# Performance work log

Hardware: AMD Instinct MI355X
Metric: run time of the kernel (lower is better)

Reference implementation:

```python
import jax, jax.numpy as jnp
import numpy as np

B, L, D, H = 4, 2048, 1024, 64  # batch, seq, d_model, head_size

def setup_inputs() -> dict:
    key = jax.random.key(0)
    k1, k2 = jax.random.split(key)
    x = jax.random.normal(k1, (B, L, D), dtype=jnp.float32)
    # nn.Linear(d_model, head_size, bias=False) weight: [head_size, d_model]
    Wq = jax.random.normal(k2, (H, D), dtype=jnp.float32) * (1.0 / np.sqrt(D))
    return {"x": x, "Wq": Wq}

def reference(x, Wq):
    # Faithful to source bug: q, k, v ALL use the query projection.
    q = jnp.einsum('bld,hd->blh', x, Wq)
    k = q
    v = q
    d_k = x.shape[-1]  # source uses d_model, not head_size
    scores = jnp.einsum('blh,bmh->blm', q, k) / jnp.sqrt(jnp.float32(d_k))
    Lq = x.shape[1]
    causal = jnp.tril(jnp.ones((Lq, Lq), dtype=bool))
    scores = jnp.where(causal, scores, -jnp.inf)
    attn = jax.nn.softmax(scores, axis=-1)
    # dropout in eval mode -> identity
    return jnp.einsum('blm,bmh->blh', attn, v)
```

## Files before the change

### kernel.cpp

```cpp
#include <hip/hip_runtime.h>
#include <cmath>

#define Bb 4
#define Ll 2048
#define Dd 1024
#define Hh 64

typedef float f32x4 __attribute__((ext_vector_type(4)));
typedef short s16x8 __attribute__((ext_vector_type(8)));

#if __has_builtin(__builtin_amdgcn_exp2f)
#define EXP2(x) __builtin_amdgcn_exp2f(x)
#else
#define EXP2(x) exp2f(x)
#endif
#define SCL 0.0450842200278f

__device__ __forceinline__ unsigned short f2bf(float f) {
    union { float f; unsigned int u; } v; v.f = f;
    unsigned int u = v.u;
    return (unsigned short)((u + 0x7FFFu + ((u >> 16) & 1u)) >> 16);
}
__device__ __forceinline__ unsigned int pack2(float a, float b) {
    return (unsigned int)f2bf(a) | ((unsigned int)f2bf(b) << 16);
}

__global__ __launch_bounds__(256) void wq_cvt(const float* __restrict__ Wq,
                                              unsigned short* __restrict__ wqb) {
    const int i = (blockIdx.x * 256 + threadIdx.x) * 8;
    float4 a = *(const float4*)(Wq + i);
    float4 b = *(const float4*)(Wq + i + 4);
    uint4 p; p.x = pack2(a.x, a.y); p.y = pack2(a.z, a.w);
    p.z = pack2(b.x, b.y); p.w = pack2(b.z, b.w);
    *(uint4*)(wqb + i) = p;
}

__global__ __launch_bounds__(128) void proj_mfma(const float* __restrict__ x,
                                                 const unsigned short* __restrict__ wqb,
                                                 unsigned short* __restrict__ q,
                                                 unsigned short* __restrict__ qT) {
    const int t = threadIdx.x;
    const int lane = t & 63;
    const int wv = t >> 6;
    const int m15 = lane & 15, q_ = lane >> 4;
    const int row0 = blockIdx.x * 32 + wv * 16;
    const float* xr = x + (size_t)(row0 + m15) * Dd + q_ * 8;

    f32x4 acc[4];
#pragma unroll
    for (int i = 0; i < 4; ++i) acc[i] = (f32x4){0.f, 0.f, 0.f, 0.f};

#pragma unroll 4
    for (int ks = 0; ks < 32; ++ks) {
        float4 a = *(const float4*)(xr + ks * 32);
        float4 b = *(const float4*)(xr + ks * 32 + 4);
        union { s16x8 v; uint4 u; } A;
        A.u.x = pack2(a.x, a.y); A.u.y = pack2(a.z, a.w);
        A.u.z = pack2(b.x, b.y); A.u.w = pack2(b.z, b.w);
#pragma unroll
        for (int ct = 0; ct < 4; ++ct) {
            s16x8 B = *(const s16x8*)(wqb + (size_t)(ct * 16 + m15) * Dd + ks * 32 + q_ * 8);
            acc[ct] = __builtin_amdgcn_mfma_f32_16x16x32_bf16(A.v, B, acc[ct], 0, 0, 0);
        }
    }
    const int b = row0 >> 11;
    const int mloc = (row0 & 2047) + q_ * 4;
#pragma unroll
    for (int ct = 0; ct < 4; ++ct) {
        const int h = ct * 16 + m15;
        unsigned short u0 = f2bf(acc[ct][0]), u1 = f2bf(acc[ct][1]);
        unsigned short u2 = f2bf(acc[ct][2]), u3 = f2bf(acc[ct][3]);
        q[(size_t)(row0 + q_ * 4 + 0) * Hh + h] = u0;
        q[(size_t)(row0 + q_ * 4 + 1) * Hh + h] = u1;
        q[(size_t)(row0 + q_ * 4 + 2) * Hh + h] = u2;
        q[(size_t)(row0 + q_ * 4 + 3) * Hh + h] = u3;
        ushort4 pk; pk.x = u0; pk.y = u1; pk.z = u2; pk.w = u3;
        *(ushort4*)&qT[((size_t)(b * Hh + h)) * Ll + mloc] = pk;
    }
}

__global__ __launch_bounds__(256, 3) void flash_mfma(const unsigned short* __restrict__ qg,
                                                     const unsigned short* __restrict__ qTg,
                                                     float* __restrict__ PO,
                                                     float* __restrict__ ML) {
    const int i = blockIdx.x;
    const int b = blockIdx.y;
    int g = (int)((sqrtf(1.0f + 2.0f * (float)i) - 1.0f) * 0.5f);
    while (2 * g * (g + 1) > i) --g;
    while (2 * (g + 1) * (g + 2) <= i) ++g;
    const int r_ = i - 2 * g * (g + 1);
    const int qt = 4 * g + r_ / (g + 1);
    const int s  = r_ % (g + 1);

    __shared__ uint4 Qs4[512], Ks4[512], Vt4[512];
    __shared__ __align__(16) unsigned short Pb[4 * 16 * 72];
    const int t = threadIdx.x, lane = t & 63, w = t >> 6;
    const int m15 = lane & 15, q_ = lane >> 4;
    const unsigned short* qb  = qg  + (size_t)b * Ll * Hh;
    const unsigned short* qTb = qTg + (size_t)b * Hh * Ll;

#pragma unroll
    for (int j = 0; j < 2; ++j) {
        int idx = t + j * 256;
        int r = idx >> 3, hc = idx & 7;
        Qs4[hc * 64 + (r ^ hc)] = *(const uint4*)(qb + (size_t)(qt * 64 + r) * Hh + hc * 8);
    }
    f32x4 Oacc[4];
#pragma unroll
    for (int k = 0; k < 4; ++k) Oacc[k] = (f32x4){0.f, 0.f, 0.f, 0.f};
    float mr = -INFINITY, lr = 0.f;
    const int n_it = min(4, qt - 4 * s + 1);
    const int c_base = s * 256;
    const int row = qt * 64 + w * 16 + m15;
    unsigned short* Pr = Pb + (w * 16 + m15) * 72;

    for (int it = 0; it < n_it; ++it) {
        const int c0 = c_base + it * 64;
        __syncthreads();
#pragma unroll
        for (int j = 0; j < 2; ++j) {
            int idx = t + j * 256;
            int c = idx >> 3, hc = idx & 7;
            Ks4[hc * 64 + (c ^ hc)] = *(const uint4*)(qb + (size_t)(c0 + c) * Hh + hc * 8);
        }
#pragma unroll
        for (int j = 0; j < 2; ++j) {
            int idx = t + j * 256;
            int h = idx >> 3, cc = idx & 7;
            Vt4[cc * 64 + (h ^ cc)] = *(const uint4*)(qTb + (size_t)h * Ll + c0 + cc * 8);
        }
        __syncthreads();
        f32x4 sc[4];
#pragma unroll
        for (int ct = 0; ct < 4; ++ct) sc[ct] = (f32x4){0.f, 0.f, 0.f, 0.f};
#pragma unroll
        for (int ks = 0; ks < 2; ++ks) {
            int hc = ks * 4 + q_;
            s16x8 Bq = *(const s16x8*)&Qs4[hc * 64 + ((w * 16 + m15) ^ hc)];
#pragma unroll
            for (int ct = 0; ct < 4; ++ct) {
                s16x8 Ak = *(const s16x8*)&Ks4[hc * 64 + ((ct * 16 + m15) ^ hc)];
                sc[ct] = __builtin_amdgcn_mfma_f32_16x16x32_bf16(Ak, Bq, sc[ct], 0, 0, 0);
            }
        }
        const bool diag = (4 * s + it) == qt;
        float v[16];
#pragma unroll
        for (int ct = 0; ct < 4; ++ct)
#pragma unroll
            for (int r = 0; r < 4; ++r) {
                float sv = sc[ct][r] * SCL;
                if (diag && (c0 + ct * 16 + q_ * 4 + r > row)) sv = -INFINITY;
                v[ct * 4 + r] = sv;
            }
        float vmax = v[0];
#pragma unroll
        for (int k = 1; k < 16; ++k) vmax = fmaxf(vmax, v[k]);
        vmax = fmaxf(vmax, __shfl_xor(vmax, 16, 64));
        vmax = fmaxf(vmax, __shfl_xor(vmax, 32, 64));
        float mnew = fmaxf(mr, vmax);
        float alpha = EXP2(mr - mnew);
        float p[16];
        float psum = 0.f;
#pragma unroll
        for (int k = 0; k < 16; ++k) { p[k] = EXP2(v[k] - mnew); psum += p[k]; }
        psum += __shfl_xor(psum, 16, 64);
        psum += __shfl_xor(psum, 32, 64);
        lr = lr * alpha + psum;
        mr = mnew;
#pragma unroll
        for (int ht = 0; ht < 4; ++ht) Oacc[ht] *= alpha;
#pragma unroll
        for (int ct = 0; ct < 4; ++ct) {
            uint2 pr; pr.x = pack2(p[ct * 4 + 0], p[ct * 4 + 1]);
            pr.y = pack2(p[ct * 4 + 2], p[ct * 4 + 3]);
            *(uint2*)(Pr + ct * 16 + q_ * 4) = pr;
        }
#pragma unroll
        for (int kc = 0; kc < 2; ++kc) {
            int cc = kc * 4 + q_;
            s16x8 Bp = *(const s16x8*)(Pr + kc * 32 + q_ * 8);
#pragma unroll
            for (int ht = 0; ht < 4; ++ht) {
                s16x8 Av = *(const s16x8*)&Vt4[cc * 64 + ((ht * 16 + m15) ^ cc)];
                Oacc[ht] = __builtin_amdgcn_mfma_f32_16x16x32_bf16(Av, Bp, Oacc[ht], 0, 0, 0);
            }
        }
    }
    const size_t base = ((size_t)((b * 32 + qt) * 8 + s)) * 4096;
#pragma unroll
    for (int ht = 0; ht < 4; ++ht)
        *(f32x4*)&PO[base + (size_t)(w * 16 + m15) * 64 + ht * 16 + q_ * 4] = Oacc[ht];
    if (q_ == 0) {
        float* mlp = ML + ((size_t)((b * 32 + qt) * 8 + s)) * 128;
        mlp[(w * 16 + m15) * 2 + 0] = mr;
        mlp[(w * 16 + m15) * 2 + 1] = lr;
    }
}

__global__ __launch_bounds__(256) void combine_k(const float* __restrict__ PO,
                                                 const float* __restrict__ ML,
                                                 float* __restrict__ out) {
    const int bq = blockIdx.x;
    const int qt = bq & 31;
    const int b = bq >> 5;
    const int ns = (qt >> 2) + 1;
    const int t = threadIdx.x;
    const int r = blockIdx.y * 32 + (t >> 3);
    const int c8 = (t & 7) * 8;
    const float* mlp = ML + (size_t)bq * 8 * 128;
    const float* pob = PO + (size_t)bq * 8 * 4096;
    float M = -INFINITY;
    for (int si = 0; si < ns; ++si) M = fmaxf(M, mlp[si * 128 + r * 2]);
    float L = 0.f;
    f32x4 a0 = {0.f, 0.f, 0.f, 0.f}, a1 = a0;
    for (int si = 0; si < ns; ++si) {
        float ms = mlp[si * 128 + r * 2], ls = mlp[si * 128 + r * 2 + 1];
        float wgt = EXP2(ms - M);
        L += ls * wgt;
        const f32x4* sp = (const f32x4*)(pob + (size_t)si * 4096 + r * 64 + c8);
        a0 += wgt * sp[0];
        a1 += wgt * sp[1];
    }
    float inv = 1.0f / L;
    f32x4* op = (f32x4*)(out + (size_t)(b * Ll + qt * 64 + r) * 64 + c8);
    op[0] = a0 * inv;
    op[1] = a1 * inv;
}

extern "C" void kernel_launch(void* const* d_in, const int* in_sizes, int n_in,
                              void* d_out, int out_size, void* d_ws, size_t ws_size,
                              hipStream_t stream) {
    const float* x  = (const float*)d_in[0];
    const float* Wq = (const float*)d_in[1];
    float* out = (float*)d_out;
    char* ws = (char*)d_ws;
    unsigned short* q   = (unsigned short*)ws;
    unsigned short* qT  = (unsigned short*)(ws + (1 << 20));
    float* PO = (float*)(ws + (2 << 20));
    float* ML = (float*)(ws + (18 << 20));
    unsigned short* wqb = (unsigned short*)(ws + (19 << 20));

    wq_cvt<<<32, 256, 0, stream>>>(Wq, wqb);
    proj_mfma<<<256, 128, 0, stream>>>(x, wqb, q, qT);
    flash_mfma<<<dim3(144, Bb), 256, 0, stream>>>(q, qT, PO, ML);
    combine_k<<<dim3(128, 2), 256, 0, stream>>>(PO, ML, out);
}
```

Baseline: 103.2 us.

## Fuse split-KV combine into flash kernel and drop Wq conversion kernel

Removes the separate Wq bf16 conversion kernel by converting Wq on the fly inside the projection kernel. Removes the combine kernel by having the last split block per query tile, found through an atomic counter, do the merge. Tiles with a single split write normalized output directly. Bf16 packing now uses the hardware-friendly __float22bfloat162_rn intrinsic. This cuts two launches and a global round trip for single-split tiles, at the cost of redundant Wq conversion in every projection block plus threadfence and atomic overhead.

Measured after the change: 202.7 us. 1.96x slower.

```diff
diff --git a/kernel.cpp b/kernel.cpp
--- a/kernel.cpp
+++ b/kernel.cpp
@@ -1,4 +1,5 @@
 #include <hip/hip_runtime.h>
+#include <hip/hip_bf16.h>
 #include <cmath>
 
 #define Bb 4
@@ -16,30 +17,25 @@
 #endif
 #define SCL 0.0450842200278f
 
+__device__ __forceinline__ unsigned int pk2(float a, float b) {
+    float2 f; f.x = a; f.y = b;
+    union { __hip_bfloat162 h; unsigned int u; } c;
+    c.h = __float22bfloat162_rn(f);
+    return c.u;
+}
 __device__ __forceinline__ unsigned short f2bf(float f) {
     union { float f; unsigned int u; } v; v.f = f;
     unsigned int u = v.u;
     return (unsigned short)((u + 0x7FFFu + ((u >> 16) & 1u)) >> 16);
 }
-__device__ __forceinline__ unsigned int pack2(float a, float b) {
-    return (unsigned int)f2bf(a) | ((unsigned int)f2bf(b) << 16);
-}
-
-__global__ __launch_bounds__(256) void wq_cvt(const float* __restrict__ Wq,
-                                              unsigned short* __restrict__ wqb) {
-    const int i = (blockIdx.x * 256 + threadIdx.x) * 8;
-    float4 a = *(const float4*)(Wq + i);
-    float4 b = *(const float4*)(Wq + i + 4);
-    uint4 p; p.x = pack2(a.x, a.y); p.y = pack2(a.z, a.w);
-    p.z = pack2(b.x, b.y); p.w = pack2(b.z, b.w);
-    *(uint4*)(wqb + i) = p;
-}
 
 __global__ __launch_bounds__(128) void proj_mfma(const float* __restrict__ x,
-                                                 const unsigned short* __restrict__ wqb,
+                                                 const float* __restrict__ Wq,
                                                  unsigned short* __restrict__ q,
-                                                 unsigned short* __restrict__ qT) {
+                                                 unsigned short* __restrict__ qT,
+                                                 int* __restrict__ cnt) {
     const int t = threadIdx.x;
+    if (blockIdx.x == 0) cnt[t] = 0;
     const int lane = t & 63;
     const int wv = t >> 6;
     const int m15 = lane & 15, q_ = lane >> 4;
@@ -55,12 +51,17 @@
         float4 a = *(const float4*)(xr + ks * 32);
         float4 b = *(const float4*)(xr + ks * 32 + 4);
         union { s16x8 v; uint4 u; } A;
-        A.u.x = pack2(a.x, a.y); A.u.y = pack2(a.z, a.w);
-        A.u.z = pack2(b.x, b.y); A.u.w = pack2(b.z, b.w);
+        A.u.x = pk2(a.x, a.y); A.u.y = pk2(a.z, a.w);
+        A.u.z = pk2(b.x, b.y); A.u.w = pk2(b.z, b.w);
 #pragma unroll
         for (int ct = 0; ct < 4; ++ct) {
-            s16x8 B = *(const s16x8*)(wqb + (size_t)(ct * 16 + m15) * Dd + ks * 32 + q_ * 8);
-            acc[ct] = __builtin_amdgcn_mfma_f32_16x16x32_bf16(A.v, B, acc[ct], 0, 0, 0);
+            const float* wr = Wq + (size_t)(ct * 16 + m15) * Dd + ks * 32 + q_ * 8;
+            float4 wa = *(const float4*)wr;
+            float4 wb = *(const float4*)(wr + 4);
+            union { s16x8 v; uint4 u; } B;
+            B.u.x = pk2(wa.x, wa.y); B.u.y = pk2(wa.z, wa.w);
+            B.u.z = pk2(wb.x, wb.y); B.u.w = pk2(wb.z, wb.w);
+            acc[ct] = __builtin_amdgcn_mfma_f32_16x16x32_bf16(A.v, B.v, acc[ct], 0, 0, 0);
         }
     }
     const int b = row0 >> 11;
@@ -82,7 +83,9 @@
 __global__ __launch_bounds__(256, 3) void flash_mfma(const unsigned short* __restrict__ qg,
                                                      const unsigned short* __restrict__ qTg,
                                                      float* __restrict__ PO,
-                                                     float* __restrict__ ML) {
+                                                     float* __restrict__ ML,
+                                                     int* __restrict__ cnt,
+                                                     float* __restrict__ out) {
     const int i = blockIdx.x;
     const int b = blockIdx.y;
     int g = (int)((sqrtf(1.0f + 2.0f * (float)i) - 1.0f) * 0.5f);
@@ -91,9 +94,11 @@
     const int r_ = i - 2 * g * (g + 1);
     const int qt = 4 * g + r_ / (g + 1);
     const int s  = r_ % (g + 1);
+    const int ns = g + 1;
 
     __shared__ uint4 Qs4[512], Ks4[512], Vt4[512];
     __shared__ __align__(16) unsigned short Pb[4 * 16 * 72];
+    __shared__ int lastFlag;
     const int t = threadIdx.x, lane = t & 63, w = t >> 6;
     const int m15 = lane & 15, q_ = lane >> 4;
     const unsigned short* qb  = qg  + (size_t)b * Ll * Hh;
@@ -172,8 +177,8 @@
         for (int ht = 0; ht < 4; ++ht) Oacc[ht] *= alpha;
 #pragma unroll
         for (int ct = 0; ct < 4; ++ct) {
-            uint2 pr; pr.x = pack2(p[ct * 4 + 0], p[ct * 4 + 1]);
-            pr.y = pack2(p[ct * 4 + 2], p[ct * 4 + 3]);
+            uint2 pr; pr.x = pk2(p[ct * 4 + 0], p[ct * 4 + 1]);
+            pr.y = pk2(p[ct * 4 + 2], p[ct * 4 + 3]);
             *(uint2*)(Pr + ct * 16 + q_ * 4) = pr;
         }
 #pragma unroll
@@ -187,45 +192,52 @@
             }
         }
     }
-    const size_t base = ((size_t)((b * 32 + qt) * 8 + s)) * 4096;
+
+    const int bq = b * 32 + qt;
+    if (ns == 1) {
+        const float inv = 1.0f / lr;
+#pragma unroll
+        for (int ht = 0; ht < 4; ++ht)
+            *(f32x4*)&out[(size_t)(b * Ll + qt * 64 + w * 16 + m15) * 64 + ht * 16 + q_ * 4]
+                = Oacc[ht] * inv;
+        return;
+    }
+    const size_t base = ((size_t)(bq * 8 + s)) * 4096;
 #pragma unroll
     for (int ht = 0; ht < 4; ++ht)
         *(f32x4*)&PO[base + (size_t)(w * 16 + m15) * 64 + ht * 16 + q_ * 4] = Oacc[ht];
     if (q_ == 0) {
-        float* mlp = ML + ((size_t)((b * 32 + qt) * 8 + s)) * 128;
+        float* mlp = ML + ((size_t)(bq * 8 + s)) * 128;
         mlp[(w * 16 + m15) * 2 + 0] = mr;
         mlp[(w * 16 + m15) * 2 + 1] = lr;
     }
-}
-
-__global__ __launch_bounds__(256) void combine_k(const float* __restrict__ PO,
-                                                 const float* __restrict__ ML,
-                                                 float* __restrict__ out) {
-    const int bq = blockIdx.x;
-    const int qt = bq & 31;
-    const int b = bq >> 5;
-    const int ns = (qt >> 2) + 1;
-    const int t = threadIdx.x;
-    const int r = blockIdx.y * 32 + (t >> 3);
-    const int c8 = (t & 7) * 8;
-    const float* mlp = ML + (size_t)bq * 8 * 128;
-    const float* pob = PO + (size_t)bq * 8 * 4096;
+    __threadfence();
+    if (t == 0) {
+        int old = __hip_atomic_fetch_add(&cnt[bq], 1, __ATOMIC_ACQ_REL,
+                                         __HIP_MEMORY_SCOPE_AGENT);
+        lastFlag = (old == ns - 1);
+    }
+    __syncthreads();
+    if (!lastFlag) return;
+    __threadfence();
+    const int r = t >> 2;
+    const int c16 = (t & 3) * 16;
+    const float* mlp = ML + (size_t)bq * 1024;
+    const float* pob = PO + (size_t)bq * 32768;
     float M = -INFINITY;
     for (int si = 0; si < ns; ++si) M = fmaxf(M, mlp[si * 128 + r * 2]);
     float L = 0.f;
-    f32x4 a0 = {0.f, 0.f, 0.f, 0.f}, a1 = a0;
+    f32x4 a0 = {0.f, 0.f, 0.f, 0.f}, a1 = a0, a2 = a0, a3 = a0;
     for (int si = 0; si < ns; ++si) {
         float ms = mlp[si * 128 + r * 2], ls = mlp[si * 128 + r * 2 + 1];
         float wgt = EXP2(ms - M);
         L += ls * wgt;
-        const f32x4* sp = (const f32x4*)(pob + (size_t)si * 4096 + r * 64 + c8);
-        a0 += wgt * sp[0];
-        a1 += wgt * sp[1];
-    }
-    float inv = 1.0f / L;
-    f32x4* op = (f32x4*)(out + (size_t)(b * Ll + qt * 64 + r) * 64 + c8);
-    op[0] = a0 * inv;
-    op[1] = a1 * inv;
+        const f32x4* sp = (const f32x4*)(pob + (size_t)si * 4096 + r * 64 + c16);
+        a0 += wgt * sp[0]; a1 += wgt * sp[1]; a2 += wgt * sp[2]; a3 += wgt * sp[3];
+    }
+    const float inv = 1.0f / L;
+    f32x4* op = (f32x4*)(out + (size_t)(b * Ll + qt * 64 + r) * 64 + c16);
+    op[0] = a0 * inv; op[1] = a1 * inv; op[2] = a2 * inv; op[3] = a3 * inv;
 }
 
 extern "C" void kernel_launch(void* const* d_in, const int* in_sizes, int n_in,
@@ -235,14 +247,12 @@
     const float* Wq = (const float*)d_in[1];
     float* out = (float*)d_out;
     char* ws = (char*)d_ws;
-    unsigned short* q   = (unsigned short*)ws;
-    unsigned short* qT  = (unsigned short*)(ws + (1 << 20));
+    unsigned short* q  = (unsigned short*)ws;
+    unsigned short* qT = (unsigned short*)(ws + (1 << 20));
     float* PO = (float*)(ws + (2 << 20));
     float* ML = (float*)(ws + (18 << 20));
-    unsigned short* wqb = (unsigned short*)(ws + (19 << 20));
-
-    wq_cvt<<<32, 256, 0, stream>>>(Wq, wqb);
-    proj_mfma<<<256, 128, 0, stream>>>(x, wqb, q, qT);
-    flash_mfma<<<dim3(144, Bb), 256, 0, stream>>>(q, qT, PO, ML);
-    combine_k<<<dim3(128, 2), 256, 0, stream>>>(PO, ML, out);
-}
+    int* cnt  = (int*)(ws + (19 << 20));
+
+    proj_mfma<<<256, 128, 0, stream>>>(x, Wq, q, qT, cnt);
+    flash_mfma<<<dim3(144, Bb), 256, 0, stream>>>(q, qT, PO, ML, cnt, out);
+}
```
